# Kernel optimization log

Hardware: AMD Instinct MI355X
Metric: run time of the kernel (lower is better)

The kernel has to match this reference:

```python
import jax, jax.numpy as jnp
import numpy as np

N_NODES = 50000


def _deg_inv_sqrt(edge_index, n):
    # GCN symmetric normalization with self-loops: deg[i] = 1 + in-degree(i)
    dst = edge_index[1]
    deg = jax.ops.segment_sum(jnp.ones(edge_index.shape[1], jnp.float32), dst, num_segments=n) + 1.0
    return deg ** -0.5


def gcn_conv(x, W, b, edge_index, dis):
    # out = D^-1/2 (A + I) D^-1/2 (x W) + b
    src, dst = edge_index[0], edge_index[1]
    h = x @ W  # [N, F_out]
    norm = dis[src] * dis[dst]  # [E]
    agg = jax.ops.segment_sum(h[src] * norm[:, None], dst, num_segments=x.shape[0])
    agg = agg + h * (dis * dis)[:, None]  # self-loop contribution
    return agg + b


def setup_inputs() -> dict:
    key = jax.random.key(0)
    ks = jax.random.split(key, 8)
    n, e, fin, fh, fo = N_NODES, 1600000, 128, 128, 64
    s = lambda f: 1.0 / np.sqrt(f)
    return {
        "x": jax.random.normal(ks[0], (n, fin), jnp.float32),
        "edge_index": jax.random.randint(ks[1], (2, e), 0, n, jnp.int64),
        "W1": jax.random.normal(ks[2], (fin, fh), jnp.float32) * s(fin),
        "b1": jnp.zeros((fh,), jnp.float32),
        "W2": jax.random.normal(ks[3], (fh, fh), jnp.float32) * s(fh),
        "b2": jnp.zeros((fh,), jnp.float32),
        "W3": jax.random.normal(ks[4], (fh, fh), jnp.float32) * s(fh),
        "b3": jnp.zeros((fh,), jnp.float32),
        "Wmu": jax.random.normal(ks[5], (fh, fo), jnp.float32) * s(fh),
        "bmu": jnp.zeros((fo,), jnp.float32),
        "Wls": jax.random.normal(ks[6], (fh, fo), jnp.float32) * s(fh),
        "bls": jnp.zeros((fo,), jnp.float32),
    }


def reference(x, edge_index, W1, b1, W2, b2, W3, b3, Wmu, bmu, Wls, bls):
    dis = _deg_inv_sqrt(edge_index, x.shape[0])
    # dropout in eval mode == identity
    h = jax.nn.relu(gcn_conv(x, W1, b1, edge_index, dis))
    h = jax.nn.relu(gcn_conv(h, W2, b2, edge_index, dis))
    h = jax.nn.relu(gcn_conv(h, W3, b3, edge_index, dis))
    mu = gcn_conv(h, Wmu, bmu, edge_index, dis)
    logstd = gcn_conv(h, Wls, bls, edge_index, dis)
    return mu, logstd
```

## Files before the change

### kernel.cpp

```cpp
#include <hip/hip_runtime.h>
#include <hip/hip_fp16.h>

#define FEAT 128
#define BKT_SHIFT 8
#define CHUNK 4096

struct half4 { __half2 lo, hi; };

__global__ __launch_bounds__(256) void k_bhist(const int* __restrict__ dstp, int E, int BL,
                                               int* __restrict__ gh) {
    __shared__ int h[256];
    int tid = threadIdx.x, b = blockIdx.x;
    h[tid] = 0;
    __syncthreads();
    int cb = b * CHUNK;
    for (int i = tid; i < CHUNK; i += 256) {
        int e = cb + i;
        if (e < E) atomicAdd(&h[dstp[e] >> BKT_SHIFT], 1);
    }
    __syncthreads();
    gh[tid * BL + b] = h[tid];
}

__global__ __launch_bounds__(256) void k_s1(const int* __restrict__ g, int len,
                                            int* __restrict__ bsum) {
    int tid = threadIdx.x;
    int i0 = blockIdx.x * 512 + tid * 2;
    int v0 = (i0 < len) ? g[i0] : 0;
    int v1 = (i0 + 1 < len) ? g[i0 + 1] : 0;
    __shared__ int s[256];
    s[tid] = v0 + v1;
    __syncthreads();
    for (int off = 128; off > 0; off >>= 1) {
        if (tid < off) s[tid] += s[tid + off];
        __syncthreads();
    }
    if (tid == 0) bsum[blockIdx.x] = s[0];
}

__global__ __launch_bounds__(256) void k_s2(int* __restrict__ bsum, int nb) {
    int tid = threadIdx.x;
    __shared__ int s[256];
    int v = (tid < nb) ? bsum[tid] : 0;
    s[tid] = v;
    __syncthreads();
    for (int off = 1; off < 256; off <<= 1) {
        int t = (tid >= off) ? s[tid - off] : 0;
        __syncthreads();
        s[tid] += t;
        __syncthreads();
    }
    if (tid < nb) bsum[tid] = s[tid] - v;
}

__global__ __launch_bounds__(256) void k_s3(const int* __restrict__ g, int len,
                                            const int* __restrict__ bsum,
                                            int* __restrict__ out) {
    int tid = threadIdx.x;
    int i0 = blockIdx.x * 512 + tid * 2;
    int v0 = (i0 < len) ? g[i0] : 0;
    int v1 = (i0 + 1 < len) ? g[i0 + 1] : 0;
    __shared__ int s[256];
    int pair = v0 + v1;
    s[tid] = pair;
    __syncthreads();
    for (int off = 1; off < 256; off <<= 1) {
        int t = (tid >= off) ? s[tid - off] : 0;
        __syncthreads();
        s[tid] += t;
        __syncthreads();
    }
    int excl = s[tid] - pair + bsum[blockIdx.x];
    if (i0 < len)     out[i0] = excl;
    if (i0 + 1 < len) out[i0 + 1] = excl + v0;
}

__global__ __launch_bounds__(256) void k_bscatter(const int* __restrict__ ei, int E, int BL,
                                                  const int* __restrict__ gscan,
                                                  int2* __restrict__ ebuf) {
    __shared__ int lcur[256];
    int tid = threadIdx.x, b = blockIdx.x;
    lcur[tid] = gscan[tid * BL + b];
    __syncthreads();
    int cb = b * CHUNK;
    for (int i = tid; i < CHUNK; i += 256) {
        int e = cb + i;
        if (e < E) {
            int s = ei[e], d = ei[E + e];
            int pos = atomicAdd(&lcur[d >> BKT_SHIFT], 1);
            ebuf[pos] = make_int2(s, d);
        }
    }
}

__global__ __launch_bounds__(256) void k_bdeg(const int2* __restrict__ ebuf,
                                              const int* __restrict__ gscan, int BL,
                                              int n, int E,
                                              int* __restrict__ row_ptr,
                                              float* __restrict__ dis) {
    __shared__ int sdeg[256], soff[256];
    int tid = threadIdx.x, k = blockIdx.x;
    int base = k << BKT_SHIFT;
    int start = gscan[k * BL];
    int end = gscan[(k + 1) * BL];
    sdeg[tid] = 0;
    __syncthreads();
    for (int e = start + tid; e < end; e += 256)
        atomicAdd(&sdeg[ebuf[e].y - base], 1);
    __syncthreads();
    int v = sdeg[tid];
    soff[tid] = v;
    __syncthreads();
    for (int off = 1; off < 256; off <<= 1) {
        int t = (tid >= off) ? soff[tid - off] : 0;
        __syncthreads();
        soff[tid] += t;
        __syncthreads();
    }
    int node = base + tid;
    if (node < n) {
        row_ptr[node] = start + soff[tid] - v;
        dis[node] = rsqrtf((float)(1 + v));
    }
    if (k == 0 && tid == 0) row_ptr[n] = E;
}

__global__ __launch_bounds__(256) void k_bfill(const int2* __restrict__ ebuf,
                                               const int* __restrict__ gscan, int BL,
                                               int n, int E,
                                               const int* __restrict__ row_ptr,
                                               const float* __restrict__ dis,
                                               int2* __restrict__ csr) {
    __shared__ int scur[256];
    int tid = threadIdx.x, k = blockIdx.x;
    int base = k << BKT_SHIFT;
    int start = gscan[k * BL];
    int end = gscan[(k + 1) * BL];
    int node = base + tid;
    scur[tid] = (node < n) ? row_ptr[node] : 0;
    __syncthreads();
    for (int e = start + tid; e < end; e += 256) {
        int2 ed = ebuf[e];
        int pos = atomicAdd(&scur[ed.y - base], 1);
        csr[pos] = make_int2(ed.x, __float_as_int(dis[ed.x] * dis[ed.y]));
    }
}

__global__ __launch_bounds__(256) void k_gemm128(const float* __restrict__ A,
                                                 const float* __restrict__ W,
                                                 float* __restrict__ out,
                                                 __half* __restrict__ out16, int n) {
    __shared__ float As[32][64];
    __shared__ float Ws[32][128];
    int tid = threadIdx.x;
    int row0b = blockIdx.x * 64;
    int tx = tid & 31, ty = tid >> 5;
    int col0 = tx * 4, r0 = ty * 8;
    float4 acc[8];
#pragma unroll
    for (int i = 0; i < 8; ++i) acc[i] = make_float4(0.f, 0.f, 0.f, 0.f);

    int sr = tid & 63;
    int sq = (tid >> 6) * 4;
    int grow = row0b + sr;

    for (int kc = 0; kc < 128; kc += 32) {
#pragma unroll
        for (int j = 0; j < 2; ++j) {
            int qk = sq + j * 16;
            float4 v = make_float4(0.f, 0.f, 0.f, 0.f);
            if (grow < n) v = *(const float4*)(A + (size_t)grow * FEAT + kc + qk);
            As[qk + 0][sr] = v.x; As[qk + 1][sr] = v.y;
            As[qk + 2][sr] = v.z; As[qk + 3][sr] = v.w;
        }
#pragma unroll
        for (int j = 0; j < 4; ++j) {
            int idx = tid + j * 256;
            int wk = idx >> 5;
            int wc = (idx & 31) * 4;
            *(float4*)&Ws[wk][wc] = *(const float4*)(W + (size_t)(kc + wk) * 128 + wc);
        }
        __syncthreads();
#pragma unroll
        for (int k = 0; k < 32; ++k) {
            float4 w = *(float4*)&Ws[k][col0];
            float a[8];
            *(float4*)&a[0] = *(float4*)&As[k][r0];
            *(float4*)&a[4] = *(float4*)&As[k][r0 + 4];
#pragma unroll
            for (int i = 0; i < 8; ++i) {
                acc[i].x += a[i] * w.x;
                acc[i].y += a[i] * w.y;
                acc[i].z += a[i] * w.z;
                acc[i].w += a[i] * w.w;
            }
        }
        __syncthreads();
    }
#pragma unroll
    for (int i = 0; i < 8; ++i) {
        int row = row0b + r0 + i;
        if (row < n) {
            *(float4*)(out + (size_t)row * 128 + col0) = acc[i];
            half4 h;
            h.lo = __floats2half2_rn(acc[i].x, acc[i].y);
            h.hi = __floats2half2_rn(acc[i].z, acc[i].w);
            *(half4*)(out16 + (size_t)row * 128 + col0) = h;
        }
    }
}

__global__ __launch_bounds__(256) void k_gemm_head(const float* __restrict__ A,
                                                   const float* __restrict__ Wmu,
                                                   const float* __restrict__ Wls,
                                                   const float* __restrict__ bmu,
                                                   const float* __restrict__ bls,
                                                   float* __restrict__ mu,
                                                   float* __restrict__ ls, int n) {
    __shared__ float As[32][64];
    __shared__ float Ws[32][128];
    int tid = threadIdx.x;
    int row0b = blockIdx.x * 64;
    int tx = tid & 31, ty = tid >> 5;
    int col0 = tx * 4, r0 = ty * 8;
    float4 acc[8];
#pragma unroll
    for (int i = 0; i < 8; ++i) acc[i] = make_float4(0.f, 0.f, 0.f, 0.f);

    int sr = tid & 63;
    int sq = (tid >> 6) * 4;
    int grow = row0b + sr;

    for (int kc = 0; kc < 128; kc += 32) {
#pragma unroll
        for (int j = 0; j < 2; ++j) {
            int qk = sq + j * 16;
            float4 v = make_float4(0.f, 0.f, 0.f, 0.f);
            if (grow < n) v = *(const float4*)(A + (size_t)grow * FEAT + kc + qk);
            As[qk + 0][sr] = v.x; As[qk + 1][sr] = v.y;
            As[qk + 2][sr] = v.z; As[qk + 3][sr] = v.w;
        }
#pragma unroll
        for (int j = 0; j < 4; ++j) {
            int idx = tid + j * 256;
            int wk = idx >> 5;
            int wc = (idx & 31) * 4;
            const float* Wp = (wc < 64) ? (Wmu + (size_t)(kc + wk) * 64 + wc)
                                        : (Wls + (size_t)(kc + wk) * 64 + (wc - 64));
            *(float4*)&Ws[wk][wc] = *(const float4*)Wp;
        }
        __syncthreads();
#pragma unroll
        for (int k = 0; k < 32; ++k) {
            float4 w = *(float4*)&Ws[k][col0];
            float a[8];
            *(float4*)&a[0] = *(float4*)&As[k][r0];
            *(float4*)&a[4] = *(float4*)&As[k][r0 + 4];
#pragma unroll
            for (int i = 0; i < 8; ++i) {
                acc[i].x += a[i] * w.x;
                acc[i].y += a[i] * w.y;
                acc[i].z += a[i] * w.z;
                acc[i].w += a[i] * w.w;
            }
        }
        __syncthreads();
    }
    bool is_mu = (col0 < 64);
    int c = is_mu ? col0 : col0 - 64;
    const float* bp = is_mu ? (bmu + c) : (bls + c);
    float4 b = *(const float4*)bp;
    float* op = is_mu ? mu : ls;
#pragma unroll
    for (int i = 0; i < 8; ++i) {
        int row = row0b + r0 + i;
        if (row < n)
            *(float4*)(op + (size_t)row * 64 + c) =
                make_float4(acc[i].x + b.x, acc[i].y + b.y, acc[i].z + b.z, acc[i].w + b.w);
    }
}

__global__ __launch_bounds__(256) void k_agg(const float* __restrict__ t32,
                                             const __half* __restrict__ t16,
                                             const int* __restrict__ row_ptr,
                                             const int2* __restrict__ csr,
                                             const float* __restrict__ dis,
                                             const float* __restrict__ bias,
                                             float* __restrict__ out,
                                             __half* __restrict__ out16,
                                             int n, int do_relu) {
    int wave = (int)((blockIdx.x * blockDim.x + threadIdx.x) >> 6);
    int lane = threadIdx.x & 63;
    if (wave >= n) return;
    int node = wave;
    float d = dis[node];
    float sw = d * d;
    size_t lo = (size_t)(lane << 1);
    float2 self = *(const float2*)(t32 + (size_t)node * FEAT + lo);
    float2 acc[8];
    acc[0].x = self.x * sw; acc[0].y = self.y * sw;
#pragma unroll
    for (int i = 1; i < 8; ++i) { acc[i].x = 0.f; acc[i].y = 0.f; }
    int e = row_ptr[node], e1 = row_ptr[node + 1];
    for (; e + 8 <= e1; e += 8) {
        int2 c[8];
#pragma unroll
        for (int i = 0; i < 8; ++i) c[i] = csr[e + i];
        __half2 hv[8];
#pragma unroll
        for (int i = 0; i < 8; ++i)
            hv[i] = *((const __half2*)(t16 + ((size_t)c[i].x << 7)) + lane);
#pragma unroll
        for (int i = 0; i < 8; ++i) {
            float w = __int_as_float(c[i].y);
            float2 v = __half22float2(hv[i]);
            acc[i].x += w * v.x;
            acc[i].y += w * v.y;
        }
    }
    for (; e + 4 <= e1; e += 4) {
        int2 c[4];
#pragma unroll
        for (int i = 0; i < 4; ++i) c[i] = csr[e + i];
#pragma unroll
        for (int i = 0; i < 4; ++i) {
            float w = __int_as_float(c[i].y);
            float2 v = __half22float2(*((const __half2*)(t16 + ((size_t)c[i].x << 7)) + lane));
            acc[i].x += w * v.x;
            acc[i].y += w * v.y;
        }
    }
    for (; e < e1; ++e) {
        int2 c0 = csr[e];
        float w0 = __int_as_float(c0.y);
        float2 v0 = __half22float2(*((const __half2*)(t16 + ((size_t)c0.x << 7)) + lane));
        acc[0].x += w0 * v0.x; acc[0].y += w0 * v0.y;
    }
#pragma unroll
    for (int i = 1; i < 8; ++i) { acc[0].x += acc[i].x; acc[0].y += acc[i].y; }
    if (bias) {
        acc[0].x += bias[lane << 1];
        acc[0].y += bias[(lane << 1) + 1];
    }
    if (do_relu) {
        acc[0].x = fmaxf(acc[0].x, 0.f);
        acc[0].y = fmaxf(acc[0].y, 0.f);
    }
    *(float2*)(out + (size_t)node * FEAT + lo) = acc[0];
    if (out16)
        *((__half2*)(out16 + (size_t)node * FEAT) + lane) = __floats2half2_rn(acc[0].x, acc[0].y);
}

extern "C" void kernel_launch(void* const* d_in, const int* in_sizes, int n_in,
                              void* d_out, int out_size, void* d_ws, size_t ws_size,
                              hipStream_t stream) {
    const float* x   = (const float*)d_in[0];
    const int*   ei  = (const int*)d_in[1];
    const float* W1  = (const float*)d_in[2];
    const float* b1  = (const float*)d_in[3];
    const float* W2  = (const float*)d_in[4];
    const float* b2  = (const float*)d_in[5];
    const float* W3  = (const float*)d_in[6];
    const float* b3  = (const float*)d_in[7];
    const float* Wmu = (const float*)d_in[8];
    const float* bmu = (const float*)d_in[9];
    const float* Wls = (const float*)d_in[10];
    const float* bls = (const float*)d_in[11];

    int n = in_sizes[0] / FEAT;
    int E = in_sizes[1] / 2;

    char* ws = (char*)d_ws;
    size_t off = 0;
    auto alloc = [&](size_t bytes) {
        void* p = ws + off;
        off = (off + bytes + 255) & ~(size_t)255;
        return p;
    };
    float*  Bt      = (float*)alloc((size_t)n * FEAT * 4);
    float*  Bh      = (float*)alloc((size_t)n * FEAT * 4);
    __half* Bt16    = (__half*)alloc((size_t)n * FEAT * 2);
    __half* Bh16    = (__half*)alloc((size_t)n * FEAT * 2);
    float*  dis     = (float*)alloc((size_t)n * 4);
    int*    row_ptr = (int*)alloc((size_t)(n + 1) * 4);
    int*    bsum    = (int*)alloc(256 * 4);
    int2*   csr     = (int2*)alloc((size_t)E * 8);

    int BL  = (E + CHUNK - 1) / CHUNK;
    int lenh = 256 * BL;
    int*    gh    = (int*)alloc((size_t)lenh * 4);
    int*    gscan = (int*)alloc((size_t)lenh * 4);
    int2*   ebuf  = (int2*)Bt;

    int NBK = (n + 255) >> BKT_SHIFT;
    int nbs = (lenh + 511) / 512;

    k_bhist<<<BL, 256, 0, stream>>>(ei + E, E, BL, gh);
    k_s1<<<nbs, 256, 0, stream>>>(gh, lenh, bsum);
    k_s2<<<1, 256, 0, stream>>>(bsum, nbs);
    k_s3<<<nbs, 256, 0, stream>>>(gh, lenh, bsum, gscan);
    k_bscatter<<<BL, 256, 0, stream>>>(ei, E, BL, gscan, ebuf);
    k_bdeg<<<NBK, 256, 0, stream>>>(ebuf, gscan, BL, n, E, row_ptr, dis);
    k_bfill<<<NBK, 256, 0, stream>>>(ebuf, gscan, BL, n, E, row_ptr, dis, csr);

    int gb = (n + 63) / 64;
    int ab = (n + 3) / 4;
    float* mu = (float*)d_out;
    float* ls = (float*)d_out + (size_t)n * 64;

    k_gemm128<<<gb, 256, 0, stream>>>(x,  W1, Bt, Bt16, n);
    k_agg<<<ab, 256, 0, stream>>>(Bt, Bt16, row_ptr, csr, dis, b1, Bh, nullptr, n, 1);
    k_gemm128<<<gb, 256, 0, stream>>>(Bh, W2, Bt, Bt16, n);
    k_agg<<<ab, 256, 0, stream>>>(Bt, Bt16, row_ptr, csr, dis, b2, Bh, nullptr, n, 1);
    k_gemm128<<<gb, 256, 0, stream>>>(Bh, W3, Bt, Bt16, n);
    k_agg<<<ab, 256, 0, stream>>>(Bt, Bt16, row_ptr, csr, dis, b3, Bh, Bh16, n, 1);
    k_agg<<<ab, 256, 0, stream>>>(Bh, Bh16, row_ptr, csr, dis, nullptr, Bt, nullptr, n, 0);
    k_gemm_head<<<gb, 256, 0, stream>>>(Bt, Wmu, Wls, bmu, bls, mu, ls, n);
}
```

Measured before the change: 507.8 us.

## Store intermediate activations in fp16 only and pre-sort edges by source

Intermediate layer activations are now kept only in fp16. The GEMMs read fp16 inputs, and the aggregation reads its self term from fp16, so the fp32 copies and their writes are gone. This roughly halves activation memory traffic between layers, at the cost of some precision in the self-loop and GEMM inputs. The edge list is also bucket-sorted by source before the stable sort by destination, so each CSR row's neighbours come out roughly ordered by source index. That ordering should improve gather locality in the aggregation kernels, but it adds an extra histogram, scan and scatter pass during preprocessing.

```diff
diff --git a/kernel.cpp b/kernel.cpp
--- a/kernel.cpp
+++ b/kernel.cpp
@@ -7,8 +7,8 @@
 
 struct half4 { __half2 lo, hi; };
 
-__global__ __launch_bounds__(256) void k_bhist(const int* __restrict__ dstp, int E, int BL,
-                                               int* __restrict__ gh) {
+__global__ __launch_bounds__(256) void k_bhist_src(const int* __restrict__ srcp, int E, int BL,
+                                                   int* __restrict__ gh) {
     __shared__ int h[256];
     int tid = threadIdx.x, b = blockIdx.x;
     h[tid] = 0;
@@ -16,7 +16,22 @@
     int cb = b * CHUNK;
     for (int i = tid; i < CHUNK; i += 256) {
         int e = cb + i;
-        if (e < E) atomicAdd(&h[dstp[e] >> BKT_SHIFT], 1);
+        if (e < E) atomicAdd(&h[srcp[e] >> BKT_SHIFT], 1);
+    }
+    __syncthreads();
+    gh[tid * BL + b] = h[tid];
+}
+
+__global__ __launch_bounds__(256) void k_bhist_dst(const int2* __restrict__ eb, int E, int BL,
+                                                   int* __restrict__ gh) {
+    __shared__ int h[256];
+    int tid = threadIdx.x, b = blockIdx.x;
+    h[tid] = 0;
+    __syncthreads();
+    int cb = b * CHUNK;
+    for (int i = tid; i < CHUNK; i += 256) {
+        int e = cb + i;
+        if (e < E) atomicAdd(&h[eb[e].y >> BKT_SHIFT], 1);
     }
     __syncthreads();
     gh[tid * BL + b] = h[tid];
@@ -75,9 +90,9 @@
     if (i0 + 1 < len) out[i0 + 1] = excl + v0;
 }
 
-__global__ __launch_bounds__(256) void k_bscatter(const int* __restrict__ ei, int E, int BL,
-                                                  const int* __restrict__ gscan,
-                                                  int2* __restrict__ ebuf) {
+__global__ __launch_bounds__(256) void k_bscat_src(const int* __restrict__ ei, int E, int BL,
+                                                   const int* __restrict__ gscan,
+                                                   int2* __restrict__ eb) {
     __shared__ int lcur[256];
     int tid = threadIdx.x, b = blockIdx.x;
     lcur[tid] = gscan[tid * BL + b];
@@ -87,8 +102,26 @@
         int e = cb + i;
         if (e < E) {
             int s = ei[e], d = ei[E + e];
-            int pos = atomicAdd(&lcur[d >> BKT_SHIFT], 1);
-            ebuf[pos] = make_int2(s, d);
+            int pos = atomicAdd(&lcur[s >> BKT_SHIFT], 1);
+            eb[pos] = make_int2(s, d);
+        }
+    }
+}
+
+__global__ __launch_bounds__(256) void k_bscat_dst(const int2* __restrict__ ebin, int E, int BL,
+                                                   const int* __restrict__ gscan,
+                                                   int2* __restrict__ ebout) {
+    __shared__ int lcur[256];
+    int tid = threadIdx.x, b = blockIdx.x;
+    lcur[tid] = gscan[tid * BL + b];
+    __syncthreads();
+    int cb = b * CHUNK;
+    for (int i = tid; i < CHUNK; i += 256) {
+        int e = cb + i;
+        if (e < E) {
+            int2 ed = ebin[e];
+            int pos = atomicAdd(&lcur[ed.y >> BKT_SHIFT], 1);
+            ebout[pos] = ed;
         }
     }
 }
@@ -146,9 +179,9 @@
     }
 }
 
-__global__ __launch_bounds__(256) void k_gemm128(const float* __restrict__ A,
+__global__ __launch_bounds__(256) void k_gemm128(const float* __restrict__ A32,
+                                                 const __half* __restrict__ A16,
                                                  const float* __restrict__ W,
-                                                 float* __restrict__ out,
                                                  __half* __restrict__ out16, int n) {
     __shared__ float As[32][64];
     __shared__ float Ws[32][128];
@@ -169,7 +202,15 @@
         for (int j = 0; j < 2; ++j) {
             int qk = sq + j * 16;
             float4 v = make_float4(0.f, 0.f, 0.f, 0.f);
-            if (grow < n) v = *(const float4*)(A + (size_t)grow * FEAT + kc + qk);
+            if (grow < n) {
+                if (A32) {
+                    v = *(const float4*)(A32 + (size_t)grow * FEAT + kc + qk);
+                } else {
+                    half4 h = *(const half4*)(A16 + (size_t)grow * FEAT + kc + qk);
+                    float2 l = __half22float2(h.lo), u = __half22float2(h.hi);
+                    v = make_float4(l.x, l.y, u.x, u.y);
+                }
+            }
             As[qk + 0][sr] = v.x; As[qk + 1][sr] = v.y;
             As[qk + 2][sr] = v.z; As[qk + 3][sr] = v.w;
         }
@@ -201,11 +242,10 @@
     for (int i = 0; i < 8; ++i) {
         int row = row0b + r0 + i;
         if (row < n) {
-            *(float4*)(out + (size_t)row * 128 + col0) = acc[i];
             half4 h;
             h.lo = __floats2half2_rn(acc[i].x, acc[i].y);
             h.hi = __floats2half2_rn(acc[i].z, acc[i].w);
-            *(half4*)(out16 + (size_t)row * 128 + col0) = h;
+            *(half4*)(out16 + (size_t)row * FEAT + col0) = h;
         }
     }
 }
@@ -280,14 +320,13 @@
     }
 }
 
-__global__ __launch_bounds__(256) void k_agg(const float* __restrict__ t32,
-                                             const __half* __restrict__ t16,
+__global__ __launch_bounds__(256) void k_agg(const __half* __restrict__ t16,
                                              const int* __restrict__ row_ptr,
                                              const int2* __restrict__ csr,
                                              const float* __restrict__ dis,
                                              const float* __restrict__ bias,
-                                             float* __restrict__ out,
                                              __half* __restrict__ out16,
+                                             float* __restrict__ out32,
                                              int n, int do_relu) {
     int wave = (int)((blockIdx.x * blockDim.x + threadIdx.x) >> 6);
     int lane = threadIdx.x & 63;
@@ -295,8 +334,7 @@
     int node = wave;
     float d = dis[node];
     float sw = d * d;
-    size_t lo = (size_t)(lane << 1);
-    float2 self = *(const float2*)(t32 + (size_t)node * FEAT + lo);
+    float2 self = __half22float2(*((const __half2*)(t16 + ((size_t)node << 7)) + lane));
     float2 acc[8];
     acc[0].x = self.x * sw; acc[0].y = self.y * sw;
 #pragma unroll
@@ -346,9 +384,10 @@
         acc[0].x = fmaxf(acc[0].x, 0.f);
         acc[0].y = fmaxf(acc[0].y, 0.f);
     }
-    *(float2*)(out + (size_t)node * FEAT + lo) = acc[0];
     if (out16)
-        *((__half2*)(out16 + (size_t)node * FEAT) + lane) = __floats2half2_rn(acc[0].x, acc[0].y);
+        *((__half2*)(out16 + ((size_t)node << 7)) + lane) = __floats2half2_rn(acc[0].x, acc[0].y);
+    if (out32)
+        *(float2*)(out32 + ((size_t)node << 7) + (lane << 1)) = acc[0];
 }
 
 extern "C" void kernel_launch(void* const* d_in, const int* in_sizes, int n_in,
@@ -377,43 +416,50 @@
         off = (off + bytes + 255) & ~(size_t)255;
         return p;
     };
-    float*  Bt      = (float*)alloc((size_t)n * FEAT * 4);
-    float*  Bh      = (float*)alloc((size_t)n * FEAT * 4);
+    float*  Bt32    = (float*)alloc((size_t)n * FEAT * 4);
     __half* Bt16    = (__half*)alloc((size_t)n * FEAT * 2);
     __half* Bh16    = (__half*)alloc((size_t)n * FEAT * 2);
     float*  dis     = (float*)alloc((size_t)n * 4);
     int*    row_ptr = (int*)alloc((size_t)(n + 1) * 4);
     int*    bsum    = (int*)alloc(256 * 4);
     int2*   csr     = (int2*)alloc((size_t)E * 8);
+    int2*   ebuf    = (int2*)alloc((size_t)E * 8);
+    int2*   ebuf2   = (int2*)alloc((size_t)E * 8);
 
     int BL  = (E + CHUNK - 1) / CHUNK;
     int lenh = 256 * BL;
-    int*    gh    = (int*)alloc((size_t)lenh * 4);
-    int*    gscan = (int*)alloc((size_t)lenh * 4);
-    int2*   ebuf  = (int2*)Bt;
+    int* gh1    = (int*)alloc((size_t)lenh * 4);
+    int* gscan1 = (int*)alloc((size_t)lenh * 4);
+    int* gh2    = (int*)alloc((size_t)lenh * 4);
+    int* gscan2 = (int*)alloc((size_t)lenh * 4);
 
     int NBK = (n + 255) >> BKT_SHIFT;
     int nbs = (lenh + 511) / 512;
 
-    k_bhist<<<BL, 256, 0, stream>>>(ei + E, E, BL, gh);
-    k_s1<<<nbs, 256, 0, stream>>>(gh, lenh, bsum);
+    k_bhist_src<<<BL, 256, 0, stream>>>(ei, E, BL, gh1);
+    k_s1<<<nbs, 256, 0, stream>>>(gh1, lenh, bsum);
     k_s2<<<1, 256, 0, stream>>>(bsum, nbs);
-    k_s3<<<nbs, 256, 0, stream>>>(gh, lenh, bsum, gscan);
-    k_bscatter<<<BL, 256, 0, stream>>>(ei, E, BL, gscan, ebuf);
-    k_bdeg<<<NBK, 256, 0, stream>>>(ebuf, gscan, BL, n, E, row_ptr, dis);
-    k_bfill<<<NBK, 256, 0, stream>>>(ebuf, gscan, BL, n, E, row_ptr, dis, csr);
+    k_s3<<<nbs, 256, 0, stream>>>(gh1, lenh, bsum, gscan1);
+    k_bscat_src<<<BL, 256, 0, stream>>>(ei, E, BL, gscan1, ebuf2);
+    k_bhist_dst<<<BL, 256, 0, stream>>>(ebuf2, E, BL, gh2);
+    k_s1<<<nbs, 256, 0, stream>>>(gh2, lenh, bsum);
+    k_s2<<<1, 256, 0, stream>>>(bsum, nbs);
+    k_s3<<<nbs, 256, 0, stream>>>(gh2, lenh, bsum, gscan2);
+    k_bscat_dst<<<BL, 256, 0, stream>>>(ebuf2, E, BL, gscan2, ebuf);
+    k_bdeg<<<NBK, 256, 0, stream>>>(ebuf, gscan2, BL, n, E, row_ptr, dis);
+    k_bfill<<<NBK, 256, 0, stream>>>(ebuf, gscan2, BL, n, E, row_ptr, dis, csr);
 
     int gb = (n + 63) / 64;
     int ab = (n + 3) / 4;
     float* mu = (float*)d_out;
     float* ls = (float*)d_out + (size_t)n * 64;
 
-    k_gemm128<<<gb, 256, 0, stream>>>(x,  W1, Bt, Bt16, n);
-    k_agg<<<ab, 256, 0, stream>>>(Bt, Bt16, row_ptr, csr, dis, b1, Bh, nullptr, n, 1);
-    k_gemm128<<<gb, 256, 0, stream>>>(Bh, W2, Bt, Bt16, n);
-    k_agg<<<ab, 256, 0, stream>>>(Bt, Bt16, row_ptr, csr, dis, b2, Bh, nullptr, n, 1);
-    k_gemm128<<<gb, 256, 0, stream>>>(Bh, W3, Bt, Bt16, n);
-    k_agg<<<ab, 256, 0, stream>>>(Bt, Bt16, row_ptr, csr, dis, b3, Bh, Bh16, n, 1);
-    k_agg<<<ab, 256, 0, stream>>>(Bh, Bh16, row_ptr, csr, dis, nullptr, Bt, nullptr, n, 0);
-    k_gemm_head<<<gb, 256, 0, stream>>>(Bt, Wmu, Wls, bmu, bls, mu, ls, n);
-}
+    k_gemm128<<<gb, 256, 0, stream>>>(x, nullptr, W1, Bt16, n);
+    k_agg<<<ab, 256, 0, stream>>>(Bt16, row_ptr, csr, dis, b1, Bh16, nullptr, n, 1);
+    k_gemm128<<<gb, 256, 0, stream>>>(nullptr, Bh16, W2, Bt16, n);
+    k_agg<<<ab, 256, 0, stream>>>(Bt16, row_ptr, csr, dis, b2, Bh16, nullptr, n, 1);
+    k_gemm128<<<gb, 256, 0, stream>>>(nullptr, Bh16, W3, Bt16, n);
+    k_agg<<<ab, 256, 0, stream>>>(Bt16, row_ptr, csr, dis, b3, Bh16, nullptr, n, 1);
+    k_agg<<<ab, 256, 0, stream>>>(Bh16, row_ptr, csr, dis, nullptr, nullptr, Bt32, n, 0);
+    k_gemm_head<<<gb, 256, 0, stream>>>(Bt32, Wmu, Wls, bmu, bls, mu, ls, n);
+}
```

Result: slower. 521.8 us (+2.8%).
